# Optimization experiments

Measured on AMD Instinct MI355X. Metric: run time of the kernel, lower is better.

Reference implementation:

```python
import jax, jax.numpy as jnp
import numpy as np

N, C_S, C_Z, H, D = 512, 384, 128, 16, 24  # c_hidden per head
EPS = 1e-5

def _ln(x, g, b):
    m = jnp.mean(x, axis=-1, keepdims=True)
    v = jnp.mean(jnp.square(x - m), axis=-1, keepdims=True)
    return (x - m) * jax.lax.rsqrt(v + EPS) * g + b

def setup_inputs() -> dict:
    key = jax.random.key(0)
    ks = jax.random.split(key, 12)
    s = lambda fan: 1.0 / np.sqrt(fan)
    return {
        "a": jax.random.normal(ks[0], (1, N, C_S), jnp.float32),
        "z": jax.random.normal(ks[1], (1, N, N, C_Z), jnp.float32),
        "g_a": jnp.ones((C_S,), jnp.float32),
        "b_a": jnp.zeros((C_S,), jnp.float32),
        "g_z": jnp.ones((C_Z,), jnp.float32),
        "b_z": jnp.zeros((C_Z,), jnp.float32),
        "Wz": jax.random.normal(ks[2], (C_Z, H), jnp.float32) * s(C_Z),
        "bz": jnp.zeros((H,), jnp.float32),
        "Wq": jax.random.normal(ks[3], (C_S, H * D), jnp.float32) * s(C_S),
        "Wk": jax.random.normal(ks[4], (C_S, H * D), jnp.float32) * s(C_S),
        "Wv": jax.random.normal(ks[5], (C_S, H * D), jnp.float32) * s(C_S),
        "Wg": jax.random.normal(ks[6], (C_S, H * D), jnp.float32) * s(C_S),
        "bg": jnp.zeros((H * D,), jnp.float32),
        "Wo": jax.random.normal(ks[7], (H * D, C_S), jnp.float32) * s(H * D),
        "bo": jnp.zeros((C_S,), jnp.float32),
    }

def reference(a, z, g_a, b_a, g_z, b_z, Wz, bz, Wq, Wk, Wv, Wg, bg, Wo, bo):
    B = a.shape[0]
    a_n = _ln(a, g_a, b_a)                       # [B,N,C_S]
    z_n = _ln(z, g_z, b_z)                       # [B,N,N,C_Z]
    # linear_z then permute(0,3,1,2): [B,N,N,H] -> [B,H,N,N]
    pair_bias = jnp.einsum('bijc,ch->bhij', z_n, Wz) + bz[None, :, None, None]
    q = (a_n @ Wq).reshape(B, N, H, D) * (1.0 / np.sqrt(D))
    k = (a_n @ Wk).reshape(B, N, H, D)
    v = (a_n @ Wv).reshape(B, N, H, D)
    scores = jnp.einsum('bqhd,bkhd->bhqk', q, k) + pair_bias
    p = jax.nn.softmax(scores, axis=-1)
    o = jnp.einsum('bhqk,bkhd->bqhd', p, v)      # [B,N,H,D]
    g = jax.nn.sigmoid(a_n @ Wg + bg).reshape(B, N, H, D)
    o = (o * g).reshape(B, N, H * D)
    return o @ Wo + bo                            # [B,N,C_S]
```

## Files before the change

### kernel.cpp

```cpp
#include <hip/hip_runtime.h>
#include <math.h>

#define N 512
#define CS 384
#define CZ 128
#define NH 16
#define DH 24
#define HD 384
#define NN (N*N)
#define EPS 1e-5f

#define OFF_AN   0
#define OFF_QT   196608
#define OFF_KT   393216
#define OFF_VT   589824
#define OFF_GT   786432
#define OFF_OG   983040
#define OFF_WZ2  1179648
#define OFF_SH   1181696
#define OFF_BH   1181712
#define OFF_BIAS 1181728

__global__ void prep_kernel(const float* __restrict__ g_z, const float* __restrict__ lnb_z,
                            const float* __restrict__ Wz, const float* __restrict__ bz,
                            float* __restrict__ ws) {
    int t = threadIdx.x;
    float* Wz2 = ws + OFF_WZ2;
    for (int i = t; i < NH * CZ; i += 256) {
        int h = i >> 7, c = i & (CZ - 1);
        Wz2[h * CZ + c] = g_z[c] * Wz[c * NH + h];
    }
    if (t < NH) {
        float s = 0.f, b = 0.f;
        for (int c = 0; c < CZ; ++c) {
            float w = Wz[c * NH + t];
            s += g_z[c] * w;
            b += lnb_z[c] * w;
        }
        ws[OFF_SH + t] = s;
        ws[OFF_BH + t] = b + bz[t];
    }
}

__global__ void ln_a_kernel(const float* __restrict__ a, const float* __restrict__ g_a,
                            const float* __restrict__ b_a, float* __restrict__ ws) {
    int r = blockIdx.x, t = threadIdx.x;
    const float* row = a + r * CS;
    float x0 = row[t], x1 = row[t + 128], x2 = row[t + 256];
    float s1 = x0 + x1 + x2;
    float s2 = x0 * x0 + x1 * x1 + x2 * x2;
    #pragma unroll
    for (int m = 1; m < 64; m <<= 1) {
        s1 += __shfl_xor(s1, m, 64);
        s2 += __shfl_xor(s2, m, 64);
    }
    __shared__ float ls1[2], ls2[2];
    if ((t & 63) == 0) { ls1[t >> 6] = s1; ls2[t >> 6] = s2; }
    __syncthreads();
    s1 = ls1[0] + ls1[1];
    s2 = ls2[0] + ls2[1];
    float mu = s1 * (1.f / CS);
    float var = s2 * (1.f / CS) - mu * mu;
    float rs = rsqrtf(var + EPS);
    float* an = ws + OFF_AN + r * CS;
    an[t]       = (x0 - mu) * rs * g_a[t]       + b_a[t];
    an[t + 128] = (x1 - mu) * rs * g_a[t + 128] + b_a[t + 128];
    an[t + 256] = (x2 - mu) * rs * g_a[t + 256] + b_a[t + 256];
}

__global__ void __launch_bounds__(256) qkvg_kernel(const float* __restrict__ Wq, const float* __restrict__ Wk,
                                                   const float* __restrict__ Wv, const float* __restrict__ Wg,
                                                   const float* __restrict__ bg, float* __restrict__ ws) {
    const int lane = threadIdx.x & 63;
    const int w = __builtin_amdgcn_readfirstlane(threadIdx.x >> 6);
    const int strip = blockIdx.x * 4 + w;
    const int n0 = strip * 16;
    const int sel = n0 / HD;
    const int col = n0 % HD;
    const float* Wm = (sel == 0) ? Wq : (sel == 1) ? Wk : (sel == 2) ? Wv : Wg;
    const int m = blockIdx.y * 64 + lane;
    const float* arow = ws + OFF_AN + m * CS;
    float acc[16];
    #pragma unroll
    for (int j = 0; j < 16; ++j) acc[j] = 0.f;
    for (int kb = 0; kb < CS; kb += 32) {
        float4 av[8];
        #pragma unroll
        for (int i = 0; i < 8; ++i) av[i] = ((const float4*)(arow + kb))[i];
        #pragma unroll
        for (int i = 0; i < 8; ++i) {
            const float* wr = Wm + (kb + i * 4) * HD + col;
            #pragma unroll
            for (int j = 0; j < 16; ++j) {
                acc[j] += av[i].x * wr[j];
                acc[j] += av[i].y * wr[HD + j];
                acc[j] += av[i].z * wr[2 * HD + j];
                acc[j] += av[i].w * wr[3 * HD + j];
            }
        }
    }
    float* dst = ws + ((sel == 0) ? OFF_QT : (sel == 1) ? OFF_KT : (sel == 2) ? OFF_VT : OFF_GT);
    if (sel == 3) {
        #pragma unroll
        for (int j = 0; j < 16; ++j) acc[j] = 1.f / (1.f + __expf(-(acc[j] + bg[col + j])));
    } else if (sel == 0) {
        #pragma unroll
        for (int j = 0; j < 16; ++j) acc[j] *= 0.20412414523193153f;
    }
    #pragma unroll
    for (int j = 0; j < 16; ++j) {
        int c = col + j;
        int h = c / DH, d = c % DH;
        dst[(h * N + m) * DH + d] = acc[j];
    }
}

__global__ void __launch_bounds__(256) pairbias_kernel(const float* __restrict__ z, float* __restrict__ ws) {
    const int row = blockIdx.x * 256 + threadIdx.x;
    const float* zr = z + (size_t)row * CZ;
    const float* Wz2 = ws + OFF_WZ2;
    float dots[NH];
    #pragma unroll
    for (int h = 0; h < NH; ++h) dots[h] = 0.f;
    float s1 = 0.f, s2 = 0.f;
    #pragma unroll
    for (int cb = 0; cb < CZ; cb += 32) {
        float4 zv[8];
        #pragma unroll
        for (int i = 0; i < 8; ++i) zv[i] = ((const float4*)(zr + cb))[i];
        #pragma unroll
        for (int i = 0; i < 8; ++i) {
            s1 += zv[i].x + zv[i].y + zv[i].z + zv[i].w;
            s2 += zv[i].x * zv[i].x + zv[i].y * zv[i].y + zv[i].z * zv[i].z + zv[i].w * zv[i].w;
            const float* wc = Wz2 + cb + i * 4;
            #pragma unroll
            for (int h = 0; h < NH; ++h) {
                dots[h] += zv[i].x * wc[h * CZ]     + zv[i].y * wc[h * CZ + 1]
                         + zv[i].z * wc[h * CZ + 2] + zv[i].w * wc[h * CZ + 3];
            }
        }
    }
    float mu = s1 * (1.f / CZ);
    float var = s2 * (1.f / CZ) - mu * mu;
    float r = rsqrtf(var + EPS);
    float* bias = ws + OFF_BIAS;
    #pragma unroll
    for (int h = 0; h < NH; ++h)
        bias[h * NN + row] = r * (dots[h] - mu * ws[OFF_SH + h]) + ws[OFF_BH + h];
}

__global__ void __launch_bounds__(256, 2) attn_kernel(float* __restrict__ ws) {
    const int lane = threadIdx.x & 63;
    const int w = __builtin_amdgcn_readfirstlane(threadIdx.x >> 6);
    const int qi = lane >> 4;
    const int klane = lane & 15;
    const int h = blockIdx.y;
    const int q = blockIdx.x * 16 + w * 4 + qi;
    const float* qT = ws + OFF_QT + h * N * DH;
    const float* kT = ws + OFF_KT + h * N * DH;
    const float* vT = ws + OFF_VT + h * N * DH;
    const float* gT = ws + OFF_GT + h * N * DH;
    const float* bias = ws + OFF_BIAS + h * NN;

    float qv[DH];
    #pragma unroll
    for (int d6 = 0; d6 < 6; ++d6) {
        float4 t4 = ((const float4*)(qT + q * DH))[d6];
        qv[d6 * 4 + 0] = t4.x; qv[d6 * 4 + 1] = t4.y; qv[d6 * 4 + 2] = t4.z; qv[d6 * 4 + 3] = t4.w;
    }
    float sc[32];
    #pragma unroll
    for (int t = 0; t < 32; ++t) {
        const int kk = t * 16 + klane;
        float kv[DH];
        #pragma unroll
        for (int d6 = 0; d6 < 6; ++d6) {
            float4 t4 = ((const float4*)(kT + kk * DH))[d6];
            kv[d6 * 4 + 0] = t4.x; kv[d6 * 4 + 1] = t4.y; kv[d6 * 4 + 2] = t4.z; kv[d6 * 4 + 3] = t4.w;
        }
        float s = 0.f;
        #pragma unroll
        for (int d = 0; d < DH; ++d) s += qv[d] * kv[d];
        sc[t] = s + bias[q * N + kk];
    }
    float mx = sc[0];
    #pragma unroll
    for (int t = 1; t < 32; ++t) mx = fmaxf(mx, sc[t]);
    #pragma unroll
    for (int m = 1; m < 16; m <<= 1) mx = fmaxf(mx, __shfl_xor(mx, m, 64));
    float sum = 0.f;
    #pragma unroll
    for (int t = 0; t < 32; ++t) { sc[t] = __expf(sc[t] - mx); sum += sc[t]; }
    #pragma unroll
    for (int m = 1; m < 16; m <<= 1) sum += __shfl_xor(sum, m, 64);
    float inv = 1.f / sum;
    #pragma unroll
    for (int t = 0; t < 32; ++t) sc[t] *= inv;
    float acc[DH];
    #pragma unroll
    for (int d = 0; d < DH; ++d) acc[d] = 0.f;
    #pragma unroll
    for (int t = 0; t < 32; ++t) {
        const int kk = t * 16 + klane;
        float vv[DH];
        #pragma unroll
        for (int d6 = 0; d6 < 6; ++d6) {
            float4 t4 = ((const float4*)(vT + kk * DH))[d6];
            vv[d6 * 4 + 0] = t4.x; vv[d6 * 4 + 1] = t4.y; vv[d6 * 4 + 2] = t4.z; vv[d6 * 4 + 3] = t4.w;
        }
        #pragma unroll
        for (int d = 0; d < DH; ++d) acc[d] += sc[t] * vv[d];
    }
    #pragma unroll
    for (int m = 1; m < 16; m <<= 1) {
        #pragma unroll
        for (int d = 0; d < DH; ++d) acc[d] += __shfl_xor(acc[d], m, 64);
    }
    float o1 = 0.f, o2 = 0.f;
    #pragma unroll
    for (int d = 0; d < 16; ++d) o1 = (klane == d) ? acc[d] : o1;
    #pragma unroll
    for (int d = 16; d < 24; ++d) o2 = (klane == (d - 16)) ? acc[d] : o2;
    float* og = ws + OFF_OG;
    og[q * HD + h * DH + klane] = o1 * gT[q * DH + klane];
    if (klane < 8)
        og[q * HD + h * DH + 16 + klane] = o2 * gT[q * DH + 16 + klane];
}

__global__ void __launch_bounds__(256) out_gemm_kernel(const float* __restrict__ Wo, const float* __restrict__ bo,
                                                       const float* __restrict__ ws, float* __restrict__ out) {
    const int lane = threadIdx.x & 63;
    const int w = __builtin_amdgcn_readfirstlane(threadIdx.x >> 6);
    const int strip = blockIdx.x * 4 + w;
    const int c0 = strip * 8;
    const int m = blockIdx.y * 64 + lane;
    const float* orow = ws + OFF_OG + m * HD;
    float acc[8];
    #pragma unroll
    for (int j = 0; j < 8; ++j) acc[j] = 0.f;
    for (int kb = 0; kb < HD; kb += 32) {
        float4 av[8];
        #pragma unroll
        for (int i = 0; i < 8; ++i) av[i] = ((const float4*)(orow + kb))[i];
        #pragma unroll
        for (int i = 0; i < 8; ++i) {
            const float* wr = Wo + (kb + i * 4) * CS + c0;
            #pragma unroll
            for (int j = 0; j < 8; ++j) {
                acc[j] += av[i].x * wr[j];
                acc[j] += av[i].y * wr[CS + j];
                acc[j] += av[i].z * wr[2 * CS + j];
                acc[j] += av[i].w * wr[3 * CS + j];
            }
        }
    }
    #pragma unroll
    for (int j = 0; j < 8; ++j) out[m * CS + c0 + j] = acc[j] + bo[c0 + j];
}

extern "C" void kernel_launch(void* const* d_in, const int* in_sizes, int n_in,
                              void* d_out, int out_size, void* d_ws, size_t ws_size,
                              hipStream_t stream) {
    const float* a    = (const float*)d_in[0];
    const float* z    = (const float*)d_in[1];
    const float* g_a  = (const float*)d_in[2];
    const float* b_a  = (const float*)d_in[3];
    const float* g_z  = (const float*)d_in[4];
    const float* b_z  = (const float*)d_in[5];
    const float* Wz   = (const float*)d_in[6];
    const float* bz   = (const float*)d_in[7];
    const float* Wq   = (const float*)d_in[8];
    const float* Wk   = (const float*)d_in[9];
    const float* Wv   = (const float*)d_in[10];
    const float* Wg   = (const float*)d_in[11];
    const float* bg   = (const float*)d_in[12];
    const float* Wo   = (const float*)d_in[13];
    const float* bo   = (const float*)d_in[14];
    float* ws  = (float*)d_ws;
    float* out = (float*)d_out;

    hipLaunchKernelGGL(prep_kernel,     dim3(1),      dim3(256), 0, stream, g_z, b_z, Wz, bz, ws);
    hipLaunchKernelGGL(ln_a_kernel,     dim3(512),    dim3(128), 0, stream, a, g_a, b_a, ws);
    hipLaunchKernelGGL(qkvg_kernel,     dim3(24, 8),  dim3(256), 0, stream, Wq, Wk, Wv, Wg, bg, ws);
    hipLaunchKernelGGL(pairbias_kernel, dim3(1024),   dim3(256), 0, stream, z, ws);
    hipLaunchKernelGGL(attn_kernel,     dim3(32, 16), dim3(256), 0, stream, ws);
    hipLaunchKernelGGL(out_gemm_kernel, dim3(12, 8),  dim3(256), 0, stream, Wo, bo, ws, out);
}
```

Measured before the change: 378.0 us.

## Split workspace into restrict pointers and rebalance all kernels for more parallelism

Each kernel now takes separate __restrict__ pointers instead of one shared workspace pointer, which lets the compiler assume no aliasing. The qkvg and output GEMMs compute narrower column strips per wave and use twice as many blocks. The attention kernel maps 32 lanes to each query instead of 16, doubling the grid and halving per-thread score registers, and drops its occupancy hint. The pair-bias loop is reordered to run per head, and the prep reduction is parallelised through shared memory. More blocks and lower register pressure are traded for more redundant loads of activation rows and longer shuffle reductions.

```diff
diff --git a/kernel.cpp b/kernel.cpp
--- a/kernel.cpp
+++ b/kernel.cpp
@@ -23,27 +23,35 @@
 
 __global__ void prep_kernel(const float* __restrict__ g_z, const float* __restrict__ lnb_z,
                             const float* __restrict__ Wz, const float* __restrict__ bz,
-                            float* __restrict__ ws) {
+                            float* __restrict__ wz2, float* __restrict__ sh, float* __restrict__ bh) {
     int t = threadIdx.x;
-    float* Wz2 = ws + OFF_WZ2;
     for (int i = t; i < NH * CZ; i += 256) {
         int h = i >> 7, c = i & (CZ - 1);
-        Wz2[h * CZ + c] = g_z[c] * Wz[c * NH + h];
-    }
+        wz2[h * CZ + c] = g_z[c] * Wz[c * NH + h];
+    }
+    __shared__ float ls[NH][17], lb[NH][17];
+    int h = t >> 4, seg = t & 15;
+    float s = 0.f, b = 0.f;
+    #pragma unroll
+    for (int i = 0; i < 8; ++i) {
+        int c = seg * 8 + i;
+        float w = Wz[c * NH + h];
+        s += g_z[c] * w;
+        b += lnb_z[c] * w;
+    }
+    ls[h][seg] = s; lb[h][seg] = b;
+    __syncthreads();
     if (t < NH) {
-        float s = 0.f, b = 0.f;
-        for (int c = 0; c < CZ; ++c) {
-            float w = Wz[c * NH + t];
-            s += g_z[c] * w;
-            b += lnb_z[c] * w;
-        }
-        ws[OFF_SH + t] = s;
-        ws[OFF_BH + t] = b + bz[t];
+        float ss = 0.f, bb = 0.f;
+        #pragma unroll
+        for (int i = 0; i < 16; ++i) { ss += ls[t][i]; bb += lb[t][i]; }
+        sh[t] = ss;
+        bh[t] = bb + bz[t];
     }
 }
 
 __global__ void ln_a_kernel(const float* __restrict__ a, const float* __restrict__ g_a,
-                            const float* __restrict__ b_a, float* __restrict__ ws) {
+                            const float* __restrict__ b_a, float* __restrict__ an_out) {
     int r = blockIdx.x, t = threadIdx.x;
     const float* row = a + r * CS;
     float x0 = row[t], x1 = row[t + 128], x2 = row[t + 256];
@@ -62,7 +70,7 @@
     float mu = s1 * (1.f / CS);
     float var = s2 * (1.f / CS) - mu * mu;
     float rs = rsqrtf(var + EPS);
-    float* an = ws + OFF_AN + r * CS;
+    float* an = an_out + r * CS;
     an[t]       = (x0 - mu) * rs * g_a[t]       + b_a[t];
     an[t + 128] = (x1 - mu) * rs * g_a[t + 128] + b_a[t + 128];
     an[t + 256] = (x2 - mu) * rs * g_a[t + 256] + b_a[t + 256];
@@ -70,19 +78,21 @@
 
 __global__ void __launch_bounds__(256) qkvg_kernel(const float* __restrict__ Wq, const float* __restrict__ Wk,
                                                    const float* __restrict__ Wv, const float* __restrict__ Wg,
-                                                   const float* __restrict__ bg, float* __restrict__ ws) {
+                                                   const float* __restrict__ bg, const float* __restrict__ an,
+                                                   float* __restrict__ qt, float* __restrict__ kt,
+                                                   float* __restrict__ vt, float* __restrict__ gt) {
     const int lane = threadIdx.x & 63;
     const int w = __builtin_amdgcn_readfirstlane(threadIdx.x >> 6);
     const int strip = blockIdx.x * 4 + w;
-    const int n0 = strip * 16;
+    const int n0 = strip * 8;
     const int sel = n0 / HD;
     const int col = n0 % HD;
     const float* Wm = (sel == 0) ? Wq : (sel == 1) ? Wk : (sel == 2) ? Wv : Wg;
     const int m = blockIdx.y * 64 + lane;
-    const float* arow = ws + OFF_AN + m * CS;
-    float acc[16];
-    #pragma unroll
-    for (int j = 0; j < 16; ++j) acc[j] = 0.f;
+    const float* arow = an + m * CS;
+    float acc[8];
+    #pragma unroll
+    for (int j = 0; j < 8; ++j) acc[j] = 0.f;
     for (int kb = 0; kb < CS; kb += 32) {
         float4 av[8];
         #pragma unroll
@@ -91,7 +101,7 @@
         for (int i = 0; i < 8; ++i) {
             const float* wr = Wm + (kb + i * 4) * HD + col;
             #pragma unroll
-            for (int j = 0; j < 16; ++j) {
+            for (int j = 0; j < 8; ++j) {
                 acc[j] += av[i].x * wr[j];
                 acc[j] += av[i].y * wr[HD + j];
                 acc[j] += av[i].z * wr[2 * HD + j];
@@ -99,26 +109,29 @@
             }
         }
     }
-    float* dst = ws + ((sel == 0) ? OFF_QT : (sel == 1) ? OFF_KT : (sel == 2) ? OFF_VT : OFF_GT);
+    float* dst = (sel == 0) ? qt : (sel == 1) ? kt : (sel == 2) ? vt : gt;
     if (sel == 3) {
         #pragma unroll
-        for (int j = 0; j < 16; ++j) acc[j] = 1.f / (1.f + __expf(-(acc[j] + bg[col + j])));
+        for (int j = 0; j < 8; ++j) acc[j] = 1.f / (1.f + __expf(-(acc[j] + bg[col + j])));
     } else if (sel == 0) {
         #pragma unroll
-        for (int j = 0; j < 16; ++j) acc[j] *= 0.20412414523193153f;
-    }
-    #pragma unroll
-    for (int j = 0; j < 16; ++j) {
+        for (int j = 0; j < 8; ++j) acc[j] *= 0.20412414523193153f;
+    }
+    #pragma unroll
+    for (int j = 0; j < 8; ++j) {
         int c = col + j;
         int h = c / DH, d = c % DH;
         dst[(h * N + m) * DH + d] = acc[j];
     }
 }
 
-__global__ void __launch_bounds__(256) pairbias_kernel(const float* __restrict__ z, float* __restrict__ ws) {
+__global__ void __launch_bounds__(256) pairbias_kernel(const float* __restrict__ z,
+                                                       const float* __restrict__ wz2,
+                                                       const float* __restrict__ sh,
+                                                       const float* __restrict__ bh,
+                                                       float* __restrict__ bias) {
     const int row = blockIdx.x * 256 + threadIdx.x;
     const float* zr = z + (size_t)row * CZ;
-    const float* Wz2 = ws + OFF_WZ2;
     float dots[NH];
     #pragma unroll
     for (int h = 0; h < NH; ++h) dots[h] = 0.f;
@@ -132,35 +145,41 @@
         for (int i = 0; i < 8; ++i) {
             s1 += zv[i].x + zv[i].y + zv[i].z + zv[i].w;
             s2 += zv[i].x * zv[i].x + zv[i].y * zv[i].y + zv[i].z * zv[i].z + zv[i].w * zv[i].w;
-            const float* wc = Wz2 + cb + i * 4;
+        }
+        #pragma unroll
+        for (int h = 0; h < NH; ++h) {
+            const float* wrow = wz2 + h * CZ + cb;
+            float d = dots[h];
             #pragma unroll
-            for (int h = 0; h < NH; ++h) {
-                dots[h] += zv[i].x * wc[h * CZ]     + zv[i].y * wc[h * CZ + 1]
-                         + zv[i].z * wc[h * CZ + 2] + zv[i].w * wc[h * CZ + 3];
+            for (int i = 0; i < 8; ++i) {
+                d += zv[i].x * wrow[i * 4 + 0];
+                d += zv[i].y * wrow[i * 4 + 1];
+                d += zv[i].z * wrow[i * 4 + 2];
+                d += zv[i].w * wrow[i * 4 + 3];
             }
+            dots[h] = d;
         }
     }
     float mu = s1 * (1.f / CZ);
     float var = s2 * (1.f / CZ) - mu * mu;
     float r = rsqrtf(var + EPS);
-    float* bias = ws + OFF_BIAS;
     #pragma unroll
     for (int h = 0; h < NH; ++h)
-        bias[h * NN + row] = r * (dots[h] - mu * ws[OFF_SH + h]) + ws[OFF_BH + h];
-}
-
-__global__ void __launch_bounds__(256, 2) attn_kernel(float* __restrict__ ws) {
+        bias[h * NN + row] = r * (dots[h] - mu * sh[h]) + bh[h];
+}
+
+__global__ void __launch_bounds__(256) attn_kernel(const float* __restrict__ qt, const float* __restrict__ kt,
+                                                   const float* __restrict__ vt, const float* __restrict__ gt,
+                                                   const float* __restrict__ bias, float* __restrict__ og) {
     const int lane = threadIdx.x & 63;
     const int w = __builtin_amdgcn_readfirstlane(threadIdx.x >> 6);
-    const int qi = lane >> 4;
-    const int klane = lane & 15;
+    const int qhalf = lane >> 5;
+    const int klane = lane & 31;
     const int h = blockIdx.y;
-    const int q = blockIdx.x * 16 + w * 4 + qi;
-    const float* qT = ws + OFF_QT + h * N * DH;
-    const float* kT = ws + OFF_KT + h * N * DH;
-    const float* vT = ws + OFF_VT + h * N * DH;
-    const float* gT = ws + OFF_GT + h * N * DH;
-    const float* bias = ws + OFF_BIAS + h * NN;
+    const int q = blockIdx.x * 8 + w * 2 + qhalf;
+    const float* qT = qt + h * N * DH;
+    const float* kT = kt + h * N * DH;
+    const float* vT = vt + h * N * DH;
 
     float qv[DH];
     #pragma unroll
@@ -168,76 +187,74 @@
         float4 t4 = ((const float4*)(qT + q * DH))[d6];
         qv[d6 * 4 + 0] = t4.x; qv[d6 * 4 + 1] = t4.y; qv[d6 * 4 + 2] = t4.z; qv[d6 * 4 + 3] = t4.w;
     }
-    float sc[32];
-    #pragma unroll
-    for (int t = 0; t < 32; ++t) {
-        const int kk = t * 16 + klane;
-        float kv[DH];
-        #pragma unroll
-        for (int d6 = 0; d6 < 6; ++d6) {
-            float4 t4 = ((const float4*)(kT + kk * DH))[d6];
-            kv[d6 * 4 + 0] = t4.x; kv[d6 * 4 + 1] = t4.y; kv[d6 * 4 + 2] = t4.z; kv[d6 * 4 + 3] = t4.w;
-        }
-        float s = 0.f;
-        #pragma unroll
-        for (int d = 0; d < DH; ++d) s += qv[d] * kv[d];
-        sc[t] = s + bias[q * N + kk];
+    float sc[16];
+    #pragma unroll
+    for (int t = 0; t < 16; ++t) {
+        const int kk = t * 32 + klane;
+        const float4* kr = (const float4*)(kT + kk * DH);
+        float4 k0 = kr[0], k1 = kr[1], k2 = kr[2], k3 = kr[3], k4 = kr[4], k5 = kr[5];
+        float s = qv[0]*k0.x + qv[1]*k0.y + qv[2]*k0.z + qv[3]*k0.w
+                + qv[4]*k1.x + qv[5]*k1.y + qv[6]*k1.z + qv[7]*k1.w
+                + qv[8]*k2.x + qv[9]*k2.y + qv[10]*k2.z + qv[11]*k2.w
+                + qv[12]*k3.x + qv[13]*k3.y + qv[14]*k3.z + qv[15]*k3.w
+                + qv[16]*k4.x + qv[17]*k4.y + qv[18]*k4.z + qv[19]*k4.w
+                + qv[20]*k5.x + qv[21]*k5.y + qv[22]*k5.z + qv[23]*k5.w;
+        sc[t] = s + bias[h * NN + q * N + kk];
     }
     float mx = sc[0];
     #pragma unroll
-    for (int t = 1; t < 32; ++t) mx = fmaxf(mx, sc[t]);
-    #pragma unroll
-    for (int m = 1; m < 16; m <<= 1) mx = fmaxf(mx, __shfl_xor(mx, m, 64));
+    for (int t = 1; t < 16; ++t) mx = fmaxf(mx, sc[t]);
+    #pragma unroll
+    for (int m = 1; m < 32; m <<= 1) mx = fmaxf(mx, __shfl_xor(mx, m, 64));
     float sum = 0.f;
     #pragma unroll
-    for (int t = 0; t < 32; ++t) { sc[t] = __expf(sc[t] - mx); sum += sc[t]; }
-    #pragma unroll
-    for (int m = 1; m < 16; m <<= 1) sum += __shfl_xor(sum, m, 64);
+    for (int t = 0; t < 16; ++t) { sc[t] = __expf(sc[t] - mx); sum += sc[t]; }
+    #pragma unroll
+    for (int m = 1; m < 32; m <<= 1) sum += __shfl_xor(sum, m, 64);
     float inv = 1.f / sum;
     #pragma unroll
-    for (int t = 0; t < 32; ++t) sc[t] *= inv;
+    for (int t = 0; t < 16; ++t) sc[t] *= inv;
     float acc[DH];
     #pragma unroll
     for (int d = 0; d < DH; ++d) acc[d] = 0.f;
     #pragma unroll
-    for (int t = 0; t < 32; ++t) {
-        const int kk = t * 16 + klane;
-        float vv[DH];
-        #pragma unroll
-        for (int d6 = 0; d6 < 6; ++d6) {
-            float4 t4 = ((const float4*)(vT + kk * DH))[d6];
-            vv[d6 * 4 + 0] = t4.x; vv[d6 * 4 + 1] = t4.y; vv[d6 * 4 + 2] = t4.z; vv[d6 * 4 + 3] = t4.w;
-        }
-        #pragma unroll
-        for (int d = 0; d < DH; ++d) acc[d] += sc[t] * vv[d];
-    }
-    #pragma unroll
-    for (int m = 1; m < 16; m <<= 1) {
+    for (int t = 0; t < 16; ++t) {
+        const int kk = t * 32 + klane;
+        const float4* vr = (const float4*)(vT + kk * DH);
+        float4 v0 = vr[0], v1 = vr[1], v2 = vr[2], v3 = vr[3], v4 = vr[4], v5 = vr[5];
+        float p = sc[t];
+        acc[0] += p*v0.x;  acc[1] += p*v0.y;  acc[2] += p*v0.z;  acc[3] += p*v0.w;
+        acc[4] += p*v1.x;  acc[5] += p*v1.y;  acc[6] += p*v1.z;  acc[7] += p*v1.w;
+        acc[8] += p*v2.x;  acc[9] += p*v2.y;  acc[10] += p*v2.z; acc[11] += p*v2.w;
+        acc[12] += p*v3.x; acc[13] += p*v3.y; acc[14] += p*v3.z; acc[15] += p*v3.w;
+        acc[16] += p*v4.x; acc[17] += p*v4.y; acc[18] += p*v4.z; acc[19] += p*v4.w;
+        acc[20] += p*v5.x; acc[21] += p*v5.y; acc[22] += p*v5.z; acc[23] += p*v5.w;
+    }
+    #pragma unroll
+    for (int m = 1; m < 32; m <<= 1) {
         #pragma unroll
         for (int d = 0; d < DH; ++d) acc[d] += __shfl_xor(acc[d], m, 64);
     }
-    float o1 = 0.f, o2 = 0.f;
-    #pragma unroll
-    for (int d = 0; d < 16; ++d) o1 = (klane == d) ? acc[d] : o1;
-    #pragma unroll
-    for (int d = 16; d < 24; ++d) o2 = (klane == (d - 16)) ? acc[d] : o2;
-    float* og = ws + OFF_OG;
-    og[q * HD + h * DH + klane] = o1 * gT[q * DH + klane];
-    if (klane < 8)
-        og[q * HD + h * DH + 16 + klane] = o2 * gT[q * DH + 16 + klane];
+    float o = 0.f;
+    #pragma unroll
+    for (int d = 0; d < DH; ++d) o = (klane == d) ? acc[d] : o;
+    if (klane < DH) {
+        float g = gt[h * N * DH + q * DH + klane];
+        og[q * HD + h * DH + klane] = o * g;
+    }
 }
 
 __global__ void __launch_bounds__(256) out_gemm_kernel(const float* __restrict__ Wo, const float* __restrict__ bo,
-                                                       const float* __restrict__ ws, float* __restrict__ out) {
+                                                       const float* __restrict__ og, float* __restrict__ out) {
     const int lane = threadIdx.x & 63;
     const int w = __builtin_amdgcn_readfirstlane(threadIdx.x >> 6);
     const int strip = blockIdx.x * 4 + w;
-    const int c0 = strip * 8;
+    const int c0 = strip * 4;
     const int m = blockIdx.y * 64 + lane;
-    const float* orow = ws + OFF_OG + m * HD;
-    float acc[8];
-    #pragma unroll
-    for (int j = 0; j < 8; ++j) acc[j] = 0.f;
+    const float* orow = og + m * HD;
+    float acc[4];
+    #pragma unroll
+    for (int j = 0; j < 4; ++j) acc[j] = 0.f;
     for (int kb = 0; kb < HD; kb += 32) {
         float4 av[8];
         #pragma unroll
@@ -246,7 +263,7 @@
         for (int i = 0; i < 8; ++i) {
             const float* wr = Wo + (kb + i * 4) * CS + c0;
             #pragma unroll
-            for (int j = 0; j < 8; ++j) {
+            for (int j = 0; j < 4; ++j) {
                 acc[j] += av[i].x * wr[j];
                 acc[j] += av[i].y * wr[CS + j];
                 acc[j] += av[i].z * wr[2 * CS + j];
@@ -255,7 +272,7 @@
         }
     }
     #pragma unroll
-    for (int j = 0; j < 8; ++j) out[m * CS + c0 + j] = acc[j] + bo[c0 + j];
+    for (int j = 0; j < 4; ++j) out[m * CS + c0 + j] = acc[j] + bo[c0 + j];
 }
 
 extern "C" void kernel_launch(void* const* d_in, const int* in_sizes, int n_in,
@@ -279,10 +296,21 @@
     float* ws  = (float*)d_ws;
     float* out = (float*)d_out;
 
-    hipLaunchKernelGGL(prep_kernel,     dim3(1),      dim3(256), 0, stream, g_z, b_z, Wz, bz, ws);
-    hipLaunchKernelGGL(ln_a_kernel,     dim3(512),    dim3(128), 0, stream, a, g_a, b_a, ws);
-    hipLaunchKernelGGL(qkvg_kernel,     dim3(24, 8),  dim3(256), 0, stream, Wq, Wk, Wv, Wg, bg, ws);
-    hipLaunchKernelGGL(pairbias_kernel, dim3(1024),   dim3(256), 0, stream, z, ws);
-    hipLaunchKernelGGL(attn_kernel,     dim3(32, 16), dim3(256), 0, stream, ws);
-    hipLaunchKernelGGL(out_gemm_kernel, dim3(12, 8),  dim3(256), 0, stream, Wo, bo, ws, out);
-}
+    float* an   = ws + OFF_AN;
+    float* qt   = ws + OFF_QT;
+    float* kt   = ws + OFF_KT;
+    float* vt   = ws + OFF_VT;
+    float* gt   = ws + OFF_GT;
+    float* ogp  = ws + OFF_OG;
+    float* wz2  = ws + OFF_WZ2;
+    float* shp  = ws + OFF_SH;
+    float* bhp  = ws + OFF_BH;
+    float* bias = ws + OFF_BIAS;
+
+    hipLaunchKernelGGL(prep_kernel,     dim3(1),      dim3(256), 0, stream, g_z, b_z, Wz, bz, wz2, shp, bhp);
+    hipLaunchKernelGGL(ln_a_kernel,     dim3(512),    dim3(128), 0, stream, a, g_a, b_a, an);
+    hipLaunchKernelGGL(qkvg_kernel,     dim3(48, 8),  dim3(256), 0, stream, Wq, Wk, Wv, Wg, bg, an, qt, kt, vt, gt);
+    hipLaunchKernelGGL(pairbias_kernel, dim3(1024),   dim3(256), 0, stream, z, wz2, shp, bhp, bias);
+    hipLaunchKernelGGL(attn_kernel,     dim3(64, 16), dim3(256), 0, stream, qt, kt, vt, gt, bias, ogp);
+    hipLaunchKernelGGL(out_gemm_kernel, dim3(24, 8),  dim3(256), 0, stream, Wo, bo, ogp, out);
+}
```

New measurement: 338.7 us. 1.12x faster.
